# Optimization experiments

Hardware: AMD Instinct MI355X
Metric: run time of the kernel (lower is better)

The kernel has to match this reference:

```python
import jax, jax.numpy as jnp
import numpy as np

N, E, HID, HEADS, KHOPS = 10000, 160000, 64, 8, 3
D = HID // HEADS  # head_dim = 8


def setup_inputs() -> dict:
    key = jax.random.key(0)
    ks = jax.random.split(key, 8)
    s = 1.0 / np.sqrt(HID)
    return {
        "x": jax.random.normal(ks[0], (N, HID), jnp.float32),
        "edge_index": jax.random.randint(ks[1], (2, E), 0, N),
        "edge_feature": jax.random.normal(ks[2], (E, HID), jnp.float32),
        "edge_weight": jax.random.uniform(ks[3], (E,), jnp.float32),
        "Wq": jax.random.normal(ks[4], (HID, HID), jnp.float32) * s,
        "bq": jnp.zeros((HID,), jnp.float32),
        "Wk": jax.random.normal(ks[5], (HID, HID), jnp.float32) * s,
        "bk": jnp.zeros((HID,), jnp.float32),
        "Wv": jax.random.normal(ks[6], (HID, HID), jnp.float32) * s,
        "bv": jnp.zeros((HID,), jnp.float32),
        "hopwise": jnp.ones((KHOPS + 1,), jnp.float32),
    }


def reference(x, edge_index, edge_feature, edge_weight, Wq, bq, Wk, bk, Wv, bv, hopwise):
    n = x.shape[0]
    row, col = edge_index[0], edge_index[1]

    # symmetric degree normalization, scaled by edge_weight
    deg = jax.ops.segment_sum(jnp.ones_like(edge_weight), col, num_segments=n)
    deg_inv = jnp.where(deg > 0, deg ** -0.5, 0.0)
    norm = deg_inv[row] * deg_inv[col] * edge_weight  # [E]

    Q = jax.nn.relu(x @ Wq + bq).reshape(n, HEADS, D)
    K = (x @ Wk + bk).reshape(n, HEADS, D)
    V = (x @ Wv + bv).reshape(n, HEADS, D)
    ef = edge_feature.reshape(-1, HEADS, D)  # [E,h,d]

    hidden = V * hopwise[0]
    sqrt_d = jnp.sqrt(jnp.asarray(D, x.dtype))

    for hop in range(KHOPS):
        if hop == 0:
            Kj = jax.nn.relu(K[row] + ef)                 # [E,h,d]
            # per-edge K (x) V outer product message, scatter-summed at col
            msg = norm[:, None, None, None] * jnp.einsum('ehi,ehj->ehij', Kj, V[row])
            M = jax.ops.segment_sum(msg, col, num_segments=n)   # [N,h,d,d]
            K = jax.ops.segment_sum(norm[:, None, None] * Kj, col, num_segments=n)
        else:
            M = jax.ops.segment_sum(norm[:, None, None, None] * M[row], col, num_segments=n)
            K = jax.ops.segment_sum(norm[:, None, None] * K[row], col, num_segments=n)

        H = jnp.einsum('nhi,nhij->nhj', Q, M)             # [N,h,d]
        nrm = jnp.sqrt(jnp.sum((H / sqrt_d) ** 2, axis=-1))  # [N,h]
        H = H / jnp.maximum(jnp.ones_like(nrm), nrm)[..., None]
        hidden = hidden + hopwise[hop + 1] * H

    return hidden.reshape(n, HEADS * D)
```

## Files before the change

### kernel.cpp

```cpp
#include <hip/hip_runtime.h>
#include <hip/hip_bf16.h>


#define HIDC 64
#define MELEMS 512

__device__ __forceinline__ unsigned bf16rne(float x) {
    unsigned u = __float_as_uint(x);
    return (u + 0x7FFFu + ((u >> 16) & 1u)) >> 16;
}
__device__ __forceinline__ unsigned pack2(float lo, float hi) {
    return bf16rne(lo) | (bf16rne(hi) << 16);
}
__device__ __forceinline__ void acc8(float* acc, float s, uint4 a) {
    acc[0] = fmaf(s, __uint_as_float(a.x << 16), acc[0]);
    acc[1] = fmaf(s, __uint_as_float(a.x & 0xFFFF0000u), acc[1]);
    acc[2] = fmaf(s, __uint_as_float(a.y << 16), acc[2]);
    acc[3] = fmaf(s, __uint_as_float(a.y & 0xFFFF0000u), acc[3]);
    acc[4] = fmaf(s, __uint_as_float(a.z << 16), acc[4]);
    acc[5] = fmaf(s, __uint_as_float(a.z & 0xFFFF0000u), acc[5]);
    acc[6] = fmaf(s, __uint_as_float(a.w << 16), acc[6]);
    acc[7] = fmaf(s, __uint_as_float(a.w & 0xFFFF0000u), acc[7]);
}

__global__ void qkv_kernel(const float* __restrict__ x,
                           const float* __restrict__ Wq, const float* __restrict__ bq,
                           const float* __restrict__ Wk, const float* __restrict__ bk,
                           const float* __restrict__ Wv, const float* __restrict__ bv,
                           const float* __restrict__ hopwise,
                           float* __restrict__ Q, float* __restrict__ K, float* __restrict__ V,
                           float* __restrict__ out, int* __restrict__ deg, int n) {
    int idx = blockIdx.x * blockDim.x + threadIdx.x;
    if (idx < n) deg[idx] = 0;
    if (idx >= n * HIDC) return;
    int node = idx >> 6, c = idx & 63;
    const float* xr = x + (size_t)node * HIDC;
    float aq = bq[c], ak = bk[c], av = bv[c];
#pragma unroll 16
    for (int k = 0; k < HIDC; ++k) {
        float xv = xr[k];
        aq = fmaf(xv, Wq[k * HIDC + c], aq);
        ak = fmaf(xv, Wk[k * HIDC + c], ak);
        av = fmaf(xv, Wv[k * HIDC + c], av);
    }
    Q[idx] = fmaxf(aq, 0.f);
    K[idx] = ak;
    V[idx] = av;
    out[idx] = hopwise[0] * av;
}

__global__ void deg_kernel(const int* __restrict__ col, int* __restrict__ deg, int e) {
    int i = blockIdx.x * blockDim.x + threadIdx.x;
    if (i < e) atomicAdd(&deg[col[i]], 1);
}

__global__ __launch_bounds__(1024) void scan_kernel(const int* __restrict__ deg,
                                                    int* __restrict__ rowptr,
                                                    int* __restrict__ cursor, int n) {
    __shared__ int wsum[16];
    __shared__ int carry;
    int tid = threadIdx.x;
    int lane = tid & 63, w = tid >> 6;
    if (tid == 0) { carry = 0; rowptr[0] = 0; }
    __syncthreads();
    for (int start = 0; start < n; start += 1024) {
        int i = start + tid;
        int v = (i < n) ? deg[i] : 0;
        int s = v;
        #pragma unroll
        for (int off = 1; off < 64; off <<= 1) {
            int t = __shfl_up(s, off);
            if (lane >= off) s += t;
        }
        if (lane == 63) wsum[w] = s;
        __syncthreads();
        if (tid == 0) {
            int acc = carry;
            #pragma unroll
            for (int w2 = 0; w2 < 16; ++w2) { int t = wsum[w2]; wsum[w2] = acc; acc += t; }
            carry = acc;
        }
        __syncthreads();
        int incl = wsum[w] + s;
        if (i < n) {
            rowptr[i + 1] = incl;
            cursor[i] = incl - v;
        }
        __syncthreads();
    }
}

__global__ void pos_kernel(const int* __restrict__ row, const int* __restrict__ col,
                           const float* __restrict__ ew, const int* __restrict__ deg,
                           int* __restrict__ cursor,
                           int* __restrict__ srcrow, float* __restrict__ snorm,
                           int* __restrict__ posarr, int e) {
    int i = blockIdx.x * blockDim.x + threadIdx.x;
    if (i >= e) return;
    int r = row[i], c = col[i];
    int dr = deg[r], dc = deg[c];
    float nv = ew[i];
    nv *= (dr > 0) ? rsqrtf((float)dr) : 0.f;
    nv *= (dc > 0) ? rsqrtf((float)dc) : 0.f;
    int pos = atomicAdd(&cursor[c], 1);
    srcrow[pos] = r;
    snorm[pos] = nv;
    posarr[i] = pos;
}

__global__ __launch_bounds__(256) void kj_kernel(
    const int* __restrict__ row, const int* __restrict__ posarr,
    const float* __restrict__ K, const float* __restrict__ ef,
    unsigned short* __restrict__ kjb, int e) {
    int gtid = blockIdx.x * blockDim.x + threadIdx.x;
    int i = gtid >> 4;
    if (i >= e) return;
    int c4 = gtid & 15;
    int lane = threadIdx.x & 63;
    int lanebase = lane & 48;
    int r = 0, pos = 0;
    if (c4 == 0) { r = row[i]; pos = posarr[i]; }
    r = __shfl(r, lanebase);
    pos = __shfl(pos, lanebase);
    const float4* efv = (const float4*)ef;
    const float4* Kv = (const float4*)K;
    float4 f = efv[(size_t)i * 16 + c4];
    float4 kk = Kv[(size_t)r * 16 + c4];
    uint2 st;
    st.x = pack2(fmaxf(kk.x + f.x, 0.f), fmaxf(kk.y + f.y, 0.f));
    st.y = pack2(fmaxf(kk.z + f.z, 0.f), fmaxf(kk.w + f.w, 0.f));
    ((uint2*)kjb)[(size_t)pos * 16 + c4] = st;
}

__device__ __forceinline__ void epilogue64(const float* acc, const float* __restrict__ Q,
                                           float hw, int n, int h, int ii,
                                           float* __restrict__ out) {
    float q = Q[n * HIDC + h * 8 + ii];
    float p[8];
    #pragma unroll
    for (int j = 0; j < 8; ++j) p[j] = q * acc[j];
    #pragma unroll
    for (int off = 1; off < 8; off <<= 1) {
        #pragma unroll
        for (int j = 0; j < 8; ++j) p[j] += __shfl_xor(p[j], off);
    }
    float ssq = 0.f;
    #pragma unroll
    for (int j = 0; j < 8; ++j) ssq = fmaf(p[j], p[j], ssq);
    float nr = sqrtf(ssq * 0.125f);
    float sc = (nr > 1.f) ? (hw / nr) : hw;
    if (ii == 0) {
        float4* o = (float4*)(out + (size_t)n * HIDC + h * 8);
        float4 c0 = o[0], c1 = o[1];
        c0.x = fmaf(p[0], sc, c0.x); c0.y = fmaf(p[1], sc, c0.y);
        c0.z = fmaf(p[2], sc, c0.z); c0.w = fmaf(p[3], sc, c0.w);
        c1.x = fmaf(p[4], sc, c1.x); c1.y = fmaf(p[5], sc, c1.y);
        c1.z = fmaf(p[6], sc, c1.z); c1.w = fmaf(p[7], sc, c1.w);
        o[0] = c0; o[1] = c1;
    }
}

__global__ __launch_bounds__(256) void hop0_kernel(
    const int* __restrict__ rowptr, const int* __restrict__ srcrow,
    const float* __restrict__ snorm, const unsigned short* __restrict__ kjb,
    const float* __restrict__ V, const float* __restrict__ Q,
    const float* __restrict__ hopwise, unsigned short* __restrict__ M0,
    float* __restrict__ out, int nn) {
    int n = blockIdx.x * 4 + (threadIdx.x >> 6);
    if (n >= nn) return;
    int t = threadIdx.x & 63;
    int h = t >> 3, ii = t & 7;
    int beg = rowptr[n], end = rowptr[n + 1];
    float acc[8] = {0, 0, 0, 0, 0, 0, 0, 0};
    const float4* Vv = (const float4*)V;
    int k = beg;
    for (; k + 2 <= end; k += 2) {
        int j0 = srcrow[k], j1 = srcrow[k + 1];
        float s0 = snorm[k] * __uint_as_float((unsigned)kjb[(size_t)k * HIDC + t] << 16);
        float s1 = snorm[k + 1] * __uint_as_float((unsigned)kjb[(size_t)(k + 1) * HIDC + t] << 16);
        float4 a0 = Vv[j0 * 16 + h * 2], b0 = Vv[j0 * 16 + h * 2 + 1];
        float4 a1 = Vv[j1 * 16 + h * 2], b1 = Vv[j1 * 16 + h * 2 + 1];
        acc[0] = fmaf(s0, a0.x, acc[0]); acc[1] = fmaf(s0, a0.y, acc[1]);
        acc[2] = fmaf(s0, a0.z, acc[2]); acc[3] = fmaf(s0, a0.w, acc[3]);
        acc[4] = fmaf(s0, b0.x, acc[4]); acc[5] = fmaf(s0, b0.y, acc[5]);
        acc[6] = fmaf(s0, b0.z, acc[6]); acc[7] = fmaf(s0, b0.w, acc[7]);
        acc[0] = fmaf(s1, a1.x, acc[0]); acc[1] = fmaf(s1, a1.y, acc[1]);
        acc[2] = fmaf(s1, a1.z, acc[2]); acc[3] = fmaf(s1, a1.w, acc[3]);
        acc[4] = fmaf(s1, b1.x, acc[4]); acc[5] = fmaf(s1, b1.y, acc[5]);
        acc[6] = fmaf(s1, b1.z, acc[6]); acc[7] = fmaf(s1, b1.w, acc[7]);
    }
    for (; k < end; ++k) {
        int j = srcrow[k];
        float s = snorm[k] * __uint_as_float((unsigned)kjb[(size_t)k * HIDC + t] << 16);
        float4 a = Vv[j * 16 + h * 2], b = Vv[j * 16 + h * 2 + 1];
        acc[0] = fmaf(s, a.x, acc[0]); acc[1] = fmaf(s, a.y, acc[1]);
        acc[2] = fmaf(s, a.z, acc[2]); acc[3] = fmaf(s, a.w, acc[3]);
        acc[4] = fmaf(s, b.x, acc[4]); acc[5] = fmaf(s, b.y, acc[5]);
        acc[6] = fmaf(s, b.z, acc[6]); acc[7] = fmaf(s, b.w, acc[7]);
    }
    uint4 st;
    st.x = pack2(acc[0], acc[1]); st.y = pack2(acc[2], acc[3]);
    st.z = pack2(acc[4], acc[5]); st.w = pack2(acc[6], acc[7]);
    ((uint4*)M0)[(size_t)n * 64 + t] = st;
    epilogue64(acc, Q, hopwise[1], n, h, ii, out);
}

__global__ __launch_bounds__(256) void hopk_kernel(
    const int* __restrict__ rowptr, const int* __restrict__ srcrow,
    const float* __restrict__ snorm, const unsigned short* __restrict__ Min,
    const float* __restrict__ Q, const float* __restrict__ hopwise, int hopidx,
    unsigned short* __restrict__ Mout, int writeM, float* __restrict__ out, int nn) {
    int n = blockIdx.x * 4 + (threadIdx.x >> 6);
    if (n >= nn) return;
    int t = threadIdx.x & 63;
    int beg = rowptr[n], end = rowptr[n + 1];
    float acc[8] = {0, 0, 0, 0, 0, 0, 0, 0};
    const uint4* Mv = (const uint4*)Min;
    int k = beg;
    for (; k + 4 <= end; k += 4) {
        int j0 = srcrow[k], j1 = srcrow[k + 1], j2 = srcrow[k + 2], j3 = srcrow[k + 3];
        float n0 = snorm[k], n1 = snorm[k + 1], n2 = snorm[k + 2], n3 = snorm[k + 3];
        uint4 a0 = Mv[(size_t)j0 * 64 + t];
        uint4 a1 = Mv[(size_t)j1 * 64 + t];
        uint4 a2 = Mv[(size_t)j2 * 64 + t];
        uint4 a3 = Mv[(size_t)j3 * 64 + t];
        acc8(acc, n0, a0);
        acc8(acc, n1, a1);
        acc8(acc, n2, a2);
        acc8(acc, n3, a3);
    }
    for (; k < end; ++k) acc8(acc, snorm[k], Mv[(size_t)srcrow[k] * 64 + t]);
    if (writeM) {
        uint4 st;
        st.x = pack2(acc[0], acc[1]); st.y = pack2(acc[2], acc[3]);
        st.z = pack2(acc[4], acc[5]); st.w = pack2(acc[6], acc[7]);
        ((uint4*)Mout)[(size_t)n * 64 + t] = st;
    }
    int h = t >> 3, ii = t & 7;
    epilogue64(acc, Q, hopwise[hopidx], n, h, ii, out);
}

extern "C" void kernel_launch(void* const* d_in, const int* in_sizes, int n_in,
                              void* d_out, int out_size, void* d_ws, size_t ws_size,
                              hipStream_t stream) {
    const float* x       = (const float*)d_in[0];
    const int*   ei      = (const int*)d_in[1];
    const float* ef      = (const float*)d_in[2];
    const float* ew      = (const float*)d_in[3];
    const float* Wq      = (const float*)d_in[4];
    const float* bq      = (const float*)d_in[5];
    const float* Wk      = (const float*)d_in[6];
    const float* bk      = (const float*)d_in[7];
    const float* Wv      = (const float*)d_in[8];
    const float* bv      = (const float*)d_in[9];
    const float* hopwise = (const float*)d_in[10];
    float* out = (float*)d_out;

    const int n = in_sizes[0] / HIDC;
    const int e = in_sizes[1] / 2;
    const int* row = ei;
    const int* col = ei + e;

    char* base = (char*)d_ws;
    size_t off = 0;
    auto alloc = [&](size_t bytes) -> void* {
        void* p = base + off;
        off = (off + bytes + 255) & ~(size_t)255;
        return p;
    };
    int*            deg    = (int*)           alloc((size_t)n * 4);
    int*            cursor = (int*)           alloc((size_t)n * 4);
    int*            rowptr = (int*)           alloc((size_t)(n + 1) * 4);
    int*            srcrow = (int*)           alloc((size_t)e * 4);
    float*          snorm  = (float*)         alloc((size_t)e * 4);
    int*            posarr = (int*)           alloc((size_t)e * 4);
    unsigned short* kjb    = (unsigned short*)alloc((size_t)e * HIDC * 2);
    float*          Q      = (float*)         alloc((size_t)n * HIDC * 4);
    float*          K      = (float*)         alloc((size_t)n * HIDC * 4);
    float*          V      = (float*)         alloc((size_t)n * HIDC * 4);
    unsigned short* M0     = (unsigned short*)alloc((size_t)n * MELEMS * 2);
    unsigned short* M1     = (unsigned short*)alloc((size_t)n * MELEMS * 2);
    (void)ws_size;

    int qb = (n * HIDC + 255) / 256;
    qkv_kernel<<<qb, 256, 0, stream>>>(x, Wq, bq, Wk, bk, Wv, bv, hopwise,
                                       Q, K, V, out, deg, n);

    int eb = (e + 255) / 256;
    deg_kernel<<<eb, 256, 0, stream>>>(col, deg, e);
    scan_kernel<<<1, 1024, 0, stream>>>(deg, rowptr, cursor, n);

    pos_kernel<<<eb, 256, 0, stream>>>(row, col, ew, deg, cursor,
                                       srcrow, snorm, posarr, e);
    int kb = ((e * 16) + 255) / 256;
    kj_kernel<<<kb, 256, 0, stream>>>(row, posarr, K, ef, kjb, e);

    int nb = (n + 3) / 4;
    hop0_kernel<<<nb, 256, 0, stream>>>(rowptr, srcrow, snorm, kjb, V, Q, hopwise, M0, out, n);
    hopk_kernel<<<nb, 256, 0, stream>>>(rowptr, srcrow, snorm, M0, Q, hopwise, 2, M1, 1, out, n);
    hopk_kernel<<<nb, 256, 0, stream>>>(rowptr, srcrow, snorm, M1, Q, hopwise, 3, M0, 0, out, n);
}
```

Measured before the change: 144.0 us.

## Fuse Kj computation into hop0 via edge-index gather, drop kj_kernel

Removes the separate kj_kernel that materialized a bf16 per-edge relu(K[row]+ef) buffer in CSR order. pos_kernel now records the original edge id per sorted slot, and hop0 gathers ef and K directly to compute Kj on the fly. This saves one launch and the write and reread of an E×64 bf16 buffer, at the cost of scattered fp32 reads of ef rows inside hop0. The QKV projection loop also now reads x as float4.

```diff
diff --git a/kernel.cpp b/kernel.cpp
--- a/kernel.cpp
+++ b/kernel.cpp
@@ -34,14 +34,24 @@
     if (idx < n) deg[idx] = 0;
     if (idx >= n * HIDC) return;
     int node = idx >> 6, c = idx & 63;
-    const float* xr = x + (size_t)node * HIDC;
+    const float4* x4 = (const float4*)(x + (size_t)node * HIDC);
     float aq = bq[c], ak = bk[c], av = bv[c];
-#pragma unroll 16
-    for (int k = 0; k < HIDC; ++k) {
-        float xv = xr[k];
-        aq = fmaf(xv, Wq[k * HIDC + c], aq);
-        ak = fmaf(xv, Wk[k * HIDC + c], ak);
-        av = fmaf(xv, Wv[k * HIDC + c], av);
+    #pragma unroll
+    for (int k4 = 0; k4 < 16; ++k4) {
+        float4 xv = x4[k4];
+        int k = k4 * 4;
+        aq = fmaf(xv.x, Wq[(k + 0) * HIDC + c], aq);
+        ak = fmaf(xv.x, Wk[(k + 0) * HIDC + c], ak);
+        av = fmaf(xv.x, Wv[(k + 0) * HIDC + c], av);
+        aq = fmaf(xv.y, Wq[(k + 1) * HIDC + c], aq);
+        ak = fmaf(xv.y, Wk[(k + 1) * HIDC + c], ak);
+        av = fmaf(xv.y, Wv[(k + 1) * HIDC + c], av);
+        aq = fmaf(xv.z, Wq[(k + 2) * HIDC + c], aq);
+        ak = fmaf(xv.z, Wk[(k + 2) * HIDC + c], ak);
+        av = fmaf(xv.z, Wv[(k + 2) * HIDC + c], av);
+        aq = fmaf(xv.w, Wq[(k + 3) * HIDC + c], aq);
+        ak = fmaf(xv.w, Wk[(k + 3) * HIDC + c], ak);
+        av = fmaf(xv.w, Wv[(k + 3) * HIDC + c], av);
     }
     Q[idx] = fmaxf(aq, 0.f);
     K[idx] = ak;
@@ -94,7 +104,7 @@
                            const float* __restrict__ ew, const int* __restrict__ deg,
                            int* __restrict__ cursor,
                            int* __restrict__ srcrow, float* __restrict__ snorm,
-                           int* __restrict__ posarr, int e) {
+                           int* __restrict__ eidx, int e) {
     int i = blockIdx.x * blockDim.x + threadIdx.x;
     if (i >= e) return;
     int r = row[i], c = col[i];
@@ -105,31 +115,7 @@
     int pos = atomicAdd(&cursor[c], 1);
     srcrow[pos] = r;
     snorm[pos] = nv;
-    posarr[i] = pos;
-}
-
-__global__ __launch_bounds__(256) void kj_kernel(
-    const int* __restrict__ row, const int* __restrict__ posarr,
-    const float* __restrict__ K, const float* __restrict__ ef,
-    unsigned short* __restrict__ kjb, int e) {
-    int gtid = blockIdx.x * blockDim.x + threadIdx.x;
-    int i = gtid >> 4;
-    if (i >= e) return;
-    int c4 = gtid & 15;
-    int lane = threadIdx.x & 63;
-    int lanebase = lane & 48;
-    int r = 0, pos = 0;
-    if (c4 == 0) { r = row[i]; pos = posarr[i]; }
-    r = __shfl(r, lanebase);
-    pos = __shfl(pos, lanebase);
-    const float4* efv = (const float4*)ef;
-    const float4* Kv = (const float4*)K;
-    float4 f = efv[(size_t)i * 16 + c4];
-    float4 kk = Kv[(size_t)r * 16 + c4];
-    uint2 st;
-    st.x = pack2(fmaxf(kk.x + f.x, 0.f), fmaxf(kk.y + f.y, 0.f));
-    st.y = pack2(fmaxf(kk.z + f.z, 0.f), fmaxf(kk.w + f.w, 0.f));
-    ((uint2*)kjb)[(size_t)pos * 16 + c4] = st;
+    eidx[pos] = i;
 }
 
 __device__ __forceinline__ void epilogue64(const float* acc, const float* __restrict__ Q,
@@ -162,7 +148,8 @@
 
 __global__ __launch_bounds__(256) void hop0_kernel(
     const int* __restrict__ rowptr, const int* __restrict__ srcrow,
-    const float* __restrict__ snorm, const unsigned short* __restrict__ kjb,
+    const float* __restrict__ snorm, const int* __restrict__ eidx,
+    const float* __restrict__ K, const float* __restrict__ ef,
     const float* __restrict__ V, const float* __restrict__ Q,
     const float* __restrict__ hopwise, unsigned short* __restrict__ M0,
     float* __restrict__ out, int nn) {
@@ -176,8 +163,11 @@
     int k = beg;
     for (; k + 2 <= end; k += 2) {
         int j0 = srcrow[k], j1 = srcrow[k + 1];
-        float s0 = snorm[k] * __uint_as_float((unsigned)kjb[(size_t)k * HIDC + t] << 16);
-        float s1 = snorm[k + 1] * __uint_as_float((unsigned)kjb[(size_t)(k + 1) * HIDC + t] << 16);
+        int e0 = eidx[k], e1 = eidx[k + 1];
+        float f0 = ef[(size_t)e0 * HIDC + t], f1 = ef[(size_t)e1 * HIDC + t];
+        float k0 = K[j0 * HIDC + t], k1 = K[j1 * HIDC + t];
+        float s0 = snorm[k] * fmaxf(k0 + f0, 0.f);
+        float s1 = snorm[k + 1] * fmaxf(k1 + f1, 0.f);
         float4 a0 = Vv[j0 * 16 + h * 2], b0 = Vv[j0 * 16 + h * 2 + 1];
         float4 a1 = Vv[j1 * 16 + h * 2], b1 = Vv[j1 * 16 + h * 2 + 1];
         acc[0] = fmaf(s0, a0.x, acc[0]); acc[1] = fmaf(s0, a0.y, acc[1]);
@@ -190,8 +180,8 @@
         acc[6] = fmaf(s1, b1.z, acc[6]); acc[7] = fmaf(s1, b1.w, acc[7]);
     }
     for (; k < end; ++k) {
-        int j = srcrow[k];
-        float s = snorm[k] * __uint_as_float((unsigned)kjb[(size_t)k * HIDC + t] << 16);
+        int j = srcrow[k], e = eidx[k];
+        float s = snorm[k] * fmaxf(K[j * HIDC + t] + ef[(size_t)e * HIDC + t], 0.f);
         float4 a = Vv[j * 16 + h * 2], b = Vv[j * 16 + h * 2 + 1];
         acc[0] = fmaf(s, a.x, acc[0]); acc[1] = fmaf(s, a.y, acc[1]);
         acc[2] = fmaf(s, a.z, acc[2]); acc[3] = fmaf(s, a.w, acc[3]);
@@ -273,8 +263,7 @@
     int*            rowptr = (int*)           alloc((size_t)(n + 1) * 4);
     int*            srcrow = (int*)           alloc((size_t)e * 4);
     float*          snorm  = (float*)         alloc((size_t)e * 4);
-    int*            posarr = (int*)           alloc((size_t)e * 4);
-    unsigned short* kjb    = (unsigned short*)alloc((size_t)e * HIDC * 2);
+    int*            eidx   = (int*)           alloc((size_t)e * 4);
     float*          Q      = (float*)         alloc((size_t)n * HIDC * 4);
     float*          K      = (float*)         alloc((size_t)n * HIDC * 4);
     float*          V      = (float*)         alloc((size_t)n * HIDC * 4);
@@ -291,12 +280,11 @@
     scan_kernel<<<1, 1024, 0, stream>>>(deg, rowptr, cursor, n);
 
     pos_kernel<<<eb, 256, 0, stream>>>(row, col, ew, deg, cursor,
-                                       srcrow, snorm, posarr, e);
-    int kb = ((e * 16) + 255) / 256;
-    kj_kernel<<<kb, 256, 0, stream>>>(row, posarr, K, ef, kjb, e);
+                                       srcrow, snorm, eidx, e);
 
     int nb = (n + 3) / 4;
-    hop0_kernel<<<nb, 256, 0, stream>>>(rowptr, srcrow, snorm, kjb, V, Q, hopwise, M0, out, n);
+    hop0_kernel<<<nb, 256, 0, stream>>>(rowptr, srcrow, snorm, eidx, K, ef, V, Q,
+                                        hopwise, M0, out, n);
     hopk_kernel<<<nb, 256, 0, stream>>>(rowptr, srcrow, snorm, M0, Q, hopwise, 2, M1, 1, out, n);
     hopk_kernel<<<nb, 256, 0, stream>>>(rowptr, srcrow, snorm, M1, Q, hopwise, 3, M0, 0, out, n);
 }
```

After: 135.5 us. 5.9% less time.
